# Optimization experiments

Hardware: AMD Instinct MI355X
Metric: run time of the kernel (lower is better)

## Reference

```python
import jax, jax.numpy as jnp
import numpy as np

B, N, D, H = 8, 2048, 128, 8
HD = D // H  # head_depth = 16
CLIP = 10.0
INF = 1e10
THETA = 10000.0
SCALE_BASE = 512.0
LOGIT_SCALE = float(np.log(400.0) / np.log(50.0) / np.sqrt(HD))


def _rotate_half(x):
    # interleaved pairs: (x1, x2) -> (-x2, x1)
    x1 = x[..., ::2]
    x2 = x[..., 1::2]
    return jnp.stack((-x2, x1), axis=-1).reshape(x.shape)


def _rope_xpos(n, hd):
    # rotary_embedding_torch RotaryEmbedding(dim=hd, use_xpos=True)
    inv_freq = 1.0 / (THETA ** (jnp.arange(0, hd, 2, dtype=jnp.float32) / hd))  # (hd/2,)
    t = jnp.arange(n, dtype=jnp.float32)
    freqs = t[:, None] * inv_freq[None, :]          # (n, hd/2)
    freqs = jnp.repeat(freqs, 2, axis=-1)           # (n, hd) interleaved dup
    sc = (jnp.arange(0, hd, 2, dtype=jnp.float32) + 0.4 * hd) / (1.4 * hd)  # (hd/2,)
    power = (t - (n // 2)) / SCALE_BASE             # centered positions
    scale = sc[None, :] ** power[:, None]           # (n, hd/2)
    scale = jnp.repeat(scale, 2, axis=-1)           # (n, hd)
    return freqs, scale


def setup_inputs() -> dict:
    key = jax.random.key(0)
    ks = jax.random.split(key, 7)
    stdv_qkv = 1.0 / np.sqrt(HD)
    stdv_out = 1.0 / np.sqrt(D)
    q = jax.random.normal(ks[0], (B, N, D), dtype=jnp.float32)
    k = jax.random.normal(ks[1], (B, N, D), dtype=jnp.float32)
    v = jax.random.normal(ks[2], (B, N, D), dtype=jnp.float32)
    Wq = jax.random.uniform(ks[3], (D, D), minval=-stdv_qkv, maxval=stdv_qkv, dtype=jnp.float32)
    Wk = jax.random.uniform(ks[4], (D, D), minval=-stdv_qkv, maxval=stdv_qkv, dtype=jnp.float32)
    Wv = jax.random.uniform(ks[5], (D, D), minval=-stdv_qkv, maxval=stdv_qkv, dtype=jnp.float32)
    Wout = jax.random.uniform(ks[6], (D, D), minval=-stdv_out, maxval=stdv_out, dtype=jnp.float32)
    mask = jnp.zeros((B, N, 1), dtype=bool)
    return {"q": q, "k": k, "v": v, "Wq": Wq, "Wk": Wk, "Wv": Wv, "Wout": Wout, "mask": mask}


def reference(q, k, v, Wq, Wk, Wv, Wout, mask):
    def split_heads(t, W):
        # torch Linear (bias=False): t @ W.T, then (B,N,H,HD) -> (B,H,N,HD)
        return (t @ W.T).reshape(B, N, H, HD).transpose(0, 2, 1, 3)

    Qh = split_heads(q, Wq)
    Kh = split_heads(k, Wk)
    Vh = split_heads(v, Wv)

    freqs, scale = _rope_xpos(N, HD)  # (N, HD) each, broadcast over (B,H,N,HD)
    cos, sin = jnp.cos(freqs), jnp.sin(freqs)
    Qr = Qh * (cos * scale) + _rotate_half(Qh) * (sin * scale)
    inv_scale = 1.0 / scale
    Kr = Kh * (cos * inv_scale) + _rotate_half(Kh) * (sin * inv_scale)

    logits = jnp.einsum('bhqd,bhkd->bhqk', Qr, Kr) * LOGIT_SCALE
    logits = CLIP * jnp.tanh(logits)
    # mask: (B,N,1) bool, True -> masked; broadcast to (B,1,1,N)
    logits = jnp.where(mask[:, None, None, :, 0], -INF, logits)
    probs = jax.nn.softmax(logits, axis=-1)
    out = jnp.einsum('bhqk,bhkd->bhqd', probs, Vh)
    out = out.transpose(0, 2, 1, 3).reshape(B, N, D)
    return out @ Wout.T
```

## Files before the change

### kernel.cpp

```cpp
#include <hip/hip_runtime.h>
#include <math.h>

#define BB 8
#define NN 2048
#define DD 128
#define HH 8

typedef _Float16 v4h __attribute__((ext_vector_type(4)));
typedef _Float16 v8h __attribute__((ext_vector_type(8)));
typedef float    v4f __attribute__((ext_vector_type(4)));
typedef float    v16f __attribute__((ext_vector_type(16)));

__device__ __forceinline__ v4f zero4() { v4f z = {0.f, 0.f, 0.f, 0.f}; return z; }
__device__ __forceinline__ v16f zero16() {
    v16f z;
    #pragma unroll
    for (int i = 0; i < 16; ++i) z[i] = 0.f;
    return z;
}

__device__ __forceinline__ v4f mfma16(v4h a, v4h b, v4f c) {
    return __builtin_amdgcn_mfma_f32_16x16x16f16(a, b, c, 0, 0, 0);
}
__device__ __forceinline__ v16f mfma32(v8h a, v8h b, v16f c) {
    return __builtin_amdgcn_mfma_f32_32x32x16_f16(a, b, c, 0, 0, 0);
}

__device__ __forceinline__ float fexp2(float x) {
#if __has_builtin(__builtin_amdgcn_exp2f)
    return __builtin_amdgcn_exp2f(x);
#else
    return __expf(x * 0.69314718055994531f);
#endif
}

#define QSCALE 1.10478088f
#define C1F 14.426950408889634f
#define C2F 28.853900817779268f

__global__ __launch_bounds__(256) void proj_rope_kernel(
    const float* __restrict__ q, const float* __restrict__ k, const float* __restrict__ v,
    const float* __restrict__ Wq, const float* __restrict__ Wk, const float* __restrict__ Wv,
    _Float16* __restrict__ Qr, _Float16* __restrict__ Kr, _Float16* __restrict__ VT)
{
    __shared__ __align__(16) _Float16 xb[64][136];
    __shared__ __align__(16) float ctc[64][16];
    __shared__ __align__(16) float cts[64][16];
    const int tid = threadIdx.x;
    const int m  = blockIdx.y;
    const int r0 = blockIdx.x * 64;
    const int b  = r0 >> 11;
    const int n0 = r0 & 2047;

    const float* s = ((m == 0) ? q : (m == 1) ? k : v) + (size_t)r0 * 128;
    #pragma unroll
    for (int i = 0; i < 8; ++i) {
        int u = tid + i * 256;
        int row = u >> 5, c4 = (u & 31) * 4;
        v4f f = *(const v4f*)(s + row * 128 + c4);
        v4h hv; hv[0]=(_Float16)f[0]; hv[1]=(_Float16)f[1]; hv[2]=(_Float16)f[2]; hv[3]=(_Float16)f[3];
        *(v4h*)&xb[row][c4] = hv;
    }

    if (m < 2) {
        #pragma unroll
        for (int i = 0; i < 2; ++i) {
            int u2 = tid + i * 256;
            int tl = u2 >> 3, j = u2 & 7;
            float fa = (j & 4) ? 1e-2f : 1.f;
            float fb = (j & 2) ? 1e-1f : 1.f;
            float fc = (j & 1) ? 0.31622776601683794f : 1.f;
            float invf = fa * fb * fc;
            float t = (float)(n0 + tl);
            float freq = t * invf;
            float c = cosf(freq), si = sinf(freq);
            float scf = ((float)(2 * j) + 6.4f) / 22.4f;
            float pw  = (t - 1024.0f) / 512.0f;
            float scl = exp2f(pw * log2f(scf));
            float sc  = (m == 0) ? scl * QSCALE : 1.0f / scl;
            float cc = c * sc, ss = si * sc;
            ctc[tl][2 * j]     = cc;
            ctc[tl][2 * j + 1] = cc;
            cts[tl][2 * j]     = ss;
            cts[tl][2 * j + 1] = ss;
        }
    }
    __syncthreads();

    const int w = tid >> 6, lane = tid & 63;
    const int l16 = lane & 15, quad = lane >> 4;

    v4h xf[8];
    #pragma unroll
    for (int kt = 0; kt < 8; ++kt)
        xf[kt] = *(const v4h*)&xb[w * 16 + l16][kt * 16 + quad * 4];
    const float* Wm = (m == 0) ? Wq : (m == 1) ? Wk : Wv;
    v4f acc[8];
    #pragma unroll
    for (int ct = 0; ct < 8; ++ct) acc[ct] = zero4();
    #pragma unroll
    for (int kt = 0; kt < 8; ++kt) {
        #pragma unroll
        for (int ct = 0; ct < 8; ++ct) {
            v4f wv = *(const v4f*)(Wm + (ct * 16 + l16) * 128 + kt * 16 + quad * 4);
            v4h wf; wf[0]=(_Float16)wv[0]; wf[1]=(_Float16)wv[1]; wf[2]=(_Float16)wv[2]; wf[3]=(_Float16)wv[3];
            if (m < 2) acc[ct] = mfma16(wf, xf[kt], acc[ct]);
            else       acc[ct] = mfma16(xf[kt], wf, acc[ct]);
        }
    }
    if (m < 2) {
        const int tl = w * 16 + l16;
        const int n = n0 + tl;
        _Float16* dst = (m == 0 ? Qr : Kr);
        #pragma unroll
        for (int ct = 0; ct < 8; ++ct) {
            v4f cs = *(const v4f*)&ctc[tl][quad * 4];
            v4f sn = *(const v4f*)&cts[tl][quad * 4];
            v4f a = acc[ct];
            v4f rot; rot[0] = -a[1]; rot[1] = a[0]; rot[2] = -a[3]; rot[3] = a[2];
            v4h o;
            #pragma unroll
            for (int r = 0; r < 4; ++r) o[r] = (_Float16)(a[r] * cs[r] + rot[r] * sn[r]);
            *(v4h*)(dst + ((size_t)(b * 8 + ct) * NN + n) * 16 + quad * 4) = o;
        }
    } else {
        #pragma unroll
        for (int ct = 0; ct < 8; ++ct) {
            v4f a = acc[ct];
            v4h o;
            #pragma unroll
            for (int r = 0; r < 4; ++r) o[r] = (_Float16)a[r];
            *(v4h*)(VT + ((size_t)(b * 8 + ct) * 16 + l16) * NN + n0 + w * 16 + quad * 4) = o;
        }
    }
}

__global__ __launch_bounds__(256, 4) void attn_kernel(
    const _Float16* __restrict__ Qr, const _Float16* __restrict__ Kr,
    const _Float16* __restrict__ VT, const unsigned char* __restrict__ mask,
    _Float16* __restrict__ Obuf)
{
    __shared__ __align__(16) char smem[30720];

    const int tid = threadIdx.x;
    const int bh = blockIdx.x >> 4;
    const int qt = blockIdx.x & 15;
    const int b = bh >> 3, h = bh & 7;
    const int q0 = qt * 128;
    const int w = tid >> 6, lane = tid & 63;
    const int l32 = lane & 31, hi = lane >> 5;

    const int qrow = q0 + w * 32 + l32;
    v8h qf = *(const v8h*)(Qr + ((size_t)bh * NN + qrow) * 16 + hi * 8);

    {
        v8h one8;
        #pragma unroll
        for (int i = 0; i < 8; ++i) one8[i] = (_Float16)1.f;
        int rr = 16 + (tid >> 4), cc = (tid & 15) * 8;
        *(v8h*)((_Float16*)(smem +         6144) + rr * 136 + cc) = one8;
        *(v8h*)((_Float16*)(smem + 15360 + 6144) + rr * 136 + cc) = one8;
    }

    v16f acc = zero16();

    const int krow = tid >> 1, kpar = tid & 1;
    const int vhd = tid >> 4, vg = tid & 15;
    const _Float16* Kbase = Kr + (size_t)bh * NN * 16;
    const _Float16* Vbase = VT + ((size_t)bh * 16 + vhd) * NN;
    const unsigned char* mbase = mask + b * NN;

    v8h kv = *(const v8h*)(Kbase + (size_t)krow * 16 + kpar * 8);
    v8h vv = *(const v8h*)(Vbase + vg * 8);
    float adv = 0.f;
    if (tid < 128) adv = mbase[tid] ? -1e30f : C1F;

    for (int it = 0; it < 16; ++it) {
        char* buf = smem + (it & 1) * 15360;
        _Float16* Kt = (_Float16*)buf;
        _Float16* Ve = (_Float16*)(buf + 6144);
        float*    av = (float*)(buf + 14848);

        *(v8h*)(Kt + krow * 24 + kpar * 8) = kv;
        {
            _Float16* vb = Ve + vhd * 136 + (vg >> 1) * 16 + (vg & 1) * 4;
            v4h lo4, hi4;
            lo4[0]=vv[0]; lo4[1]=vv[1]; lo4[2]=vv[2]; lo4[3]=vv[3];
            hi4[0]=vv[4]; hi4[1]=vv[5]; hi4[2]=vv[6]; hi4[3]=vv[7];
            *(v4h*)(vb)     = lo4;
            *(v4h*)(vb + 8) = hi4;
        }
        if (tid < 128) av[tid] = adv;
        if (it < 15) {
            const int k0n = (it + 1) * 128;
            kv = *(const v8h*)(Kbase + (size_t)(k0n + krow) * 16 + kpar * 8);
            vv = *(const v8h*)(Vbase + k0n + vg * 8);
            if (tid < 128) adv = mbase[k0n + tid] ? -1e30f : C1F;
        }
        __syncthreads();

        #pragma unroll
        for (int kc = 0; kc < 4; ++kc) {
            v8h kf = *(const v8h*)(Kt + (kc * 32 + l32) * 24 + hi * 8);
            v16f sv = mfma32(kf, qf, zero16());

            v4f ad[4];
            #pragma unroll
            for (int gg = 0; gg < 4; ++gg)
                ad[gg] = *(const v4f*)(av + kc * 32 + gg * 8 + hi * 4);

            float p[16];
            #pragma unroll
            for (int r = 0; r < 16; ++r) {
                float u  = fexp2(sv[r]);
                float rc = __builtin_amdgcn_rcpf(u + 1.f);
                p[r] = fexp2(__builtin_fmaf(rc, -C2F, ad[r >> 2][r & 3]));
            }

            #pragma unroll
            for (int c2 = 0; c2 < 2; ++c2) {
                v8h pa;
                #pragma unroll
                for (int j = 0; j < 8; ++j) pa[j] = (_Float16)p[c2 * 8 + j];
                v8h vf = *(const v8h*)(Ve + l32 * 136 + (kc * 2 + c2) * 16 + hi * 8);
                acc = mfma32(pa, vf, acc);
            }
        }
    }

    float rs[16];
    #pragma unroll
    for (int r = 0; r < 16; ++r) rs[r] = __shfl_xor(acc[r], 16, 64);

    _Float16* myOt = (_Float16*)smem + w * 768;
    if (!(lane & 16)) {
        int j = lane & 15;
        #pragma unroll
        for (int r = 0; r < 16; ++r) {
            int qr = (r & 3) + 8 * (r >> 2) + 4 * hi;
            myOt[qr * 24 + j] = (_Float16)(acc[r] * __builtin_amdgcn_rcpf(rs[r]));
        }
    }
    asm volatile("s_waitcnt lgkmcnt(0)" ::: "memory");
    v8h ov = *(const v8h*)(myOt + (lane >> 1) * 24 + (lane & 1) * 8);
    *(v8h*)(Obuf + ((size_t)(b * NN + q0 + w * 32 + (lane >> 1)) * 128) + h * 16 + (lane & 1) * 8) = ov;
}

__global__ __launch_bounds__(256) void outproj_kernel(
    const _Float16* __restrict__ Obuf, const float* __restrict__ Wo,
    float* __restrict__ out)
{
    __shared__ __align__(16) _Float16 ob[64][136];
    const int tid = threadIdx.x;
    const int r0 = blockIdx.x * 64;
    const int ct0 = blockIdx.y * 2;
    #pragma unroll
    for (int i = 0; i < 8; ++i) {
        int u = tid + i * 256;
        int row = u >> 5, c4 = (u & 31) * 4;
        *(v4h*)&ob[row][c4] = *(const v4h*)(Obuf + (size_t)(r0 + row) * 128 + c4);
    }
    __syncthreads();
    const int w = tid >> 6, lane = tid & 63;
    const int l16 = lane & 15, quad = lane >> 4;
    v4h af[8];
    #pragma unroll
    for (int kt = 0; kt < 8; ++kt)
        af[kt] = *(const v4h*)&ob[w * 16 + l16][kt * 16 + quad * 4];
    v4f acc[2];
    #pragma unroll
    for (int c = 0; c < 2; ++c) acc[c] = zero4();
    #pragma unroll
    for (int kt = 0; kt < 8; ++kt)
        #pragma unroll
        for (int c = 0; c < 2; ++c) {
            v4f wv = *(const v4f*)(Wo + ((ct0 + c) * 16 + l16) * 128 + kt * 16 + quad * 4);
            v4h wf; wf[0]=(_Float16)wv[0]; wf[1]=(_Float16)wv[1]; wf[2]=(_Float16)wv[2]; wf[3]=(_Float16)wv[3];
            acc[c] = mfma16(af[kt], wf, acc[c]);
        }
    #pragma unroll
    for (int c = 0; c < 2; ++c)
        #pragma unroll
        for (int r = 0; r < 4; ++r)
            out[(size_t)(r0 + w * 16 + quad * 4 + r) * 128 + (ct0 + c) * 16 + l16] = acc[c][r];
}

extern "C" void kernel_launch(void* const* d_in, const int* in_sizes, int n_in,
                              void* d_out, int out_size, void* d_ws, size_t ws_size,
                              hipStream_t stream)
{
    const float* q  = (const float*)d_in[0];
    const float* k  = (const float*)d_in[1];
    const float* v  = (const float*)d_in[2];
    const float* Wq = (const float*)d_in[3];
    const float* Wk = (const float*)d_in[4];
    const float* Wv = (const float*)d_in[5];
    const float* Wo = (const float*)d_in[6];
    const unsigned char* mask = (const unsigned char*)d_in[7];
    float* out = (float*)d_out;

    char* ws = (char*)d_ws;
    _Float16* Qr   = (_Float16*)(ws);
    _Float16* Kr   = (_Float16*)(ws + 4194304);
    _Float16* VTd  = (_Float16*)(ws + 8388608);
    _Float16* Obuf = (_Float16*)(ws + 12582912);

    proj_rope_kernel<<<dim3(256, 3), 256, 0, stream>>>(q, k, v, Wq, Wk, Wv, Qr, Kr, VTd);
    attn_kernel<<<1024, 256, 0, stream>>>(Qr, Kr, VTd, mask, Obuf);
    outproj_kernel<<<dim3(256, 4), 256, 0, stream>>>(Obuf, Wo, out);
}
```

Before: 195.1 us.

## Load K/V fragments directly from global memory and skip mask reads when unmasked

Removes the LDS staging and double buffering of K, V and mask tiles in the attention kernel. Each wave now loads its MFMA operand fragments straight from global memory (relying on cache), with V written in a permuted column order by the projection kernel so fragments are contiguous. A wave-level ballot precomputes which 32-key chunks contain any masked key, so per-element mask reads are skipped for fully unmasked tiles. Block indices are also remapped so that blocks sharing the same head run together, to improve L2 reuse. The risk is higher global-load latency with no explicit prefetch or overlap, now that the __syncthreads-based pipeline is gone.

Result: slower. 204.3 us (+4.7%).

```diff
diff --git a/kernel.cpp b/kernel.cpp
--- a/kernel.cpp
+++ b/kernel.cpp
@@ -124,13 +124,14 @@
             *(v4h*)(dst + ((size_t)(b * 8 + ct) * NN + n) * 16 + quad * 4) = o;
         }
     } else {
+        const int quadp = (quad == 1) ? 2 : (quad == 2) ? 1 : quad;
         #pragma unroll
         for (int ct = 0; ct < 8; ++ct) {
             v4f a = acc[ct];
             v4h o;
             #pragma unroll
             for (int r = 0; r < 4; ++r) o[r] = (_Float16)a[r];
-            *(v4h*)(VT + ((size_t)(b * 8 + ct) * 16 + l16) * NN + n0 + w * 16 + quad * 4) = o;
+            *(v4h*)(VT + ((size_t)(b * 8 + ct) * 16 + l16) * NN + n0 + w * 16 + quadp * 4) = o;
         }
     }
 }
@@ -140,91 +141,75 @@
     const _Float16* __restrict__ VT, const unsigned char* __restrict__ mask,
     _Float16* __restrict__ Obuf)
 {
-    __shared__ __align__(16) char smem[30720];
-
-    const int tid = threadIdx.x;
-    const int bh = blockIdx.x >> 4;
-    const int qt = blockIdx.x & 15;
+    __shared__ __align__(16) _Float16 osm[4 * 768];
+
+    const int raw = blockIdx.x;
+    const int lb  = (raw & 7) * 128 + (raw >> 3);
+    const int bh = lb >> 4;
+    const int qt = lb & 15;
     const int b = bh >> 3, h = bh & 7;
     const int q0 = qt * 128;
+    const int tid = threadIdx.x;
     const int w = tid >> 6, lane = tid & 63;
     const int l32 = lane & 31, hi = lane >> 5;
 
     const int qrow = q0 + w * 32 + l32;
     v8h qf = *(const v8h*)(Qr + ((size_t)bh * NN + qrow) * 16 + hi * 8);
 
+    v8h one8;
+    #pragma unroll
+    for (int i = 0; i < 8; ++i) one8[i] = (_Float16)1.f;
+
+    unsigned long long any4;
     {
-        v8h one8;
-        #pragma unroll
-        for (int i = 0; i < 8; ++i) one8[i] = (_Float16)1.f;
-        int rr = 16 + (tid >> 4), cc = (tid & 15) * 8;
-        *(v8h*)((_Float16*)(smem +         6144) + rr * 136 + cc) = one8;
-        *(v8h*)((_Float16*)(smem + 15360 + 6144) + rr * 136 + cc) = one8;
+        const unsigned long long* mq = (const unsigned long long*)(mask + (size_t)b * NN);
+        unsigned long long m0 = mq[lane * 4] | mq[lane * 4 + 1] | mq[lane * 4 + 2] | mq[lane * 4 + 3];
+        any4 = __ballot(m0 != 0);
     }
 
     v16f acc = zero16();
-
-    const int krow = tid >> 1, kpar = tid & 1;
-    const int vhd = tid >> 4, vg = tid & 15;
-    const _Float16* Kbase = Kr + (size_t)bh * NN * 16;
-    const _Float16* Vbase = VT + ((size_t)bh * 16 + vhd) * NN;
-    const unsigned char* mbase = mask + b * NN;
-
-    v8h kv = *(const v8h*)(Kbase + (size_t)krow * 16 + kpar * 8);
-    v8h vv = *(const v8h*)(Vbase + vg * 8);
-    float adv = 0.f;
-    if (tid < 128) adv = mbase[tid] ? -1e30f : C1F;
-
+    const _Float16* Kb = Kr + (size_t)bh * NN * 16;
+    const _Float16* Vb = VT + ((size_t)bh * 16 + l32) * NN;
+
+    #pragma unroll 1
     for (int it = 0; it < 16; ++it) {
-        char* buf = smem + (it & 1) * 15360;
-        _Float16* Kt = (_Float16*)buf;
-        _Float16* Ve = (_Float16*)(buf + 6144);
-        float*    av = (float*)(buf + 14848);
-
-        *(v8h*)(Kt + krow * 24 + kpar * 8) = kv;
-        {
-            _Float16* vb = Ve + vhd * 136 + (vg >> 1) * 16 + (vg & 1) * 4;
-            v4h lo4, hi4;
-            lo4[0]=vv[0]; lo4[1]=vv[1]; lo4[2]=vv[2]; lo4[3]=vv[3];
-            hi4[0]=vv[4]; hi4[1]=vv[5]; hi4[2]=vv[6]; hi4[3]=vv[7];
-            *(v4h*)(vb)     = lo4;
-            *(v4h*)(vb + 8) = hi4;
-        }
-        if (tid < 128) av[tid] = adv;
-        if (it < 15) {
-            const int k0n = (it + 1) * 128;
-            kv = *(const v8h*)(Kbase + (size_t)(k0n + krow) * 16 + kpar * 8);
-            vv = *(const v8h*)(Vbase + k0n + vg * 8);
-            if (tid < 128) adv = mbase[k0n + tid] ? -1e30f : C1F;
-        }
-        __syncthreads();
+        const int k0 = it * 128;
+        const bool mt = ((any4 >> (it * 4)) & 15ull) != 0;
 
         #pragma unroll
         for (int kc = 0; kc < 4; ++kc) {
-            v8h kf = *(const v8h*)(Kt + (kc * 32 + l32) * 24 + hi * 8);
+            v8h kf = *(const v8h*)(Kb + (size_t)(k0 + kc * 32 + l32) * 16 + hi * 8);
+            v8h vfa = one8, vfb = one8;
+            if (l32 < 16) {
+                vfa = *(const v8h*)(Vb + k0 + kc * 32 + hi * 8);
+                vfb = *(const v8h*)(Vb + k0 + kc * 32 + 16 + hi * 8);
+            }
             v16f sv = mfma32(kf, qf, zero16());
 
-            v4f ad[4];
-            #pragma unroll
-            for (int gg = 0; gg < 4; ++gg)
-                ad[gg] = *(const v4f*)(av + kc * 32 + gg * 8 + hi * 4);
+            float ad[16];
+            if (mt) {
+                #pragma unroll
+                for (int r = 0; r < 16; ++r) {
+                    int kk = k0 + kc * 32 + (r >> 2) * 8 + hi * 4 + (r & 3);
+                    ad[r] = mask[(size_t)b * NN + kk] ? -1e30f : C1F;
+                }
+            } else {
+                #pragma unroll
+                for (int r = 0; r < 16; ++r) ad[r] = C1F;
+            }
 
             float p[16];
             #pragma unroll
             for (int r = 0; r < 16; ++r) {
                 float u  = fexp2(sv[r]);
                 float rc = __builtin_amdgcn_rcpf(u + 1.f);
-                p[r] = fexp2(__builtin_fmaf(rc, -C2F, ad[r >> 2][r & 3]));
+                p[r] = fexp2(__builtin_fmaf(rc, -C2F, ad[r]));
             }
-
-            #pragma unroll
-            for (int c2 = 0; c2 < 2; ++c2) {
-                v8h pa;
-                #pragma unroll
-                for (int j = 0; j < 8; ++j) pa[j] = (_Float16)p[c2 * 8 + j];
-                v8h vf = *(const v8h*)(Ve + l32 * 136 + (kc * 2 + c2) * 16 + hi * 8);
-                acc = mfma32(pa, vf, acc);
-            }
+            v8h pa0, pa1;
+            #pragma unroll
+            for (int j = 0; j < 8; ++j) { pa0[j] = (_Float16)p[j]; pa1[j] = (_Float16)p[8 + j]; }
+            acc = mfma32(pa0, vfa, acc);
+            acc = mfma32(pa1, vfb, acc);
         }
     }
 
@@ -232,7 +217,7 @@
     #pragma unroll
     for (int r = 0; r < 16; ++r) rs[r] = __shfl_xor(acc[r], 16, 64);
 
-    _Float16* myOt = (_Float16*)smem + w * 768;
+    _Float16* myOt = osm + w * 768;
     if (!(lane & 16)) {
         int j = lane & 15;
         #pragma unroll
```
